# Kernel tuning notes

Hardware: AMD Instinct MI355X
Metric: run time of the kernel (lower is better)

## Reference

```python
import jax, jax.numpy as jnp
import numpy as np

B, L, T, D, F = 8, 12, 36, 1024, 3  # batch, local len, hist samples (n*tau), nodes, features
C = 32  # c_out


def setup_inputs() -> dict:
    key = jax.random.key(0)
    ks = jax.random.split(key, 8)
    s = 1.0 / np.sqrt(F)  # conv fan-in init scale
    return {
        "x_local": jax.random.normal(ks[0], (B, L, D, F), jnp.float32),
        "x_hist": jax.random.normal(ks[1], (B, L, T, D, F), jnp.float32),
        "Wq": jax.random.normal(ks[2], (C, F), jnp.float32) * s,
        "bq": jax.random.normal(ks[3], (C,), jnp.float32) * s,
        "Wm": jax.random.normal(ks[4], (C, F), jnp.float32) * s,
        "bm": jax.random.normal(ks[5], (C,), jnp.float32) * s,
        "Wc": jax.random.normal(ks[6], (C, F), jnp.float32) * s,
        "bc": jax.random.normal(ks[7], (C,), jnp.float32) * s,
    }


def reference(x_local, x_hist, Wq, bq, Wm, bm, Wc, bc):
    # 1x1 Conv2d/Conv3d over the feature channel F == pointwise linear in f.
    # torch permutes are absorbed into einsum axis ordering.
    q = jnp.einsum('bldf,cf->bcld', x_local, Wq) + bq[None, :, None, None]        # (B,C,L,D)
    m = jnp.einsum('bltdf,cf->bcltd', x_hist, Wm) + bm[None, :, None, None, None]  # (B,C,L,T,D)
    c = jnp.einsum('bltdf,cf->bcltd', x_hist, Wc) + bc[None, :, None, None, None]  # (B,C,L,T,D)
    mq = jnp.einsum('bcltd,bcld->bclt', m, q)                                     # scores (B,C,L,T)
    att = jax.nn.softmax(jax.nn.relu(mq), axis=-1)
    o = jnp.einsum('bclt,bcltd->bcld', att, c)                                    # memory read (B,C,L,D)
    return q + o
```

## Files before the change

kernel.cpp:

```cpp
#include <hip/hip_runtime.h>
#include <math.h>

#define BB 8
#define LL 12
#define TT 36
#define DD 1024
#define CC 32

__global__ __launch_bounds__(64) void k_Z(const float* __restrict__ xl,
                                          const float* __restrict__ xh,
                                          float* __restrict__ Zg) {
  const int blk  = blockIdx.x;
  const int bl   = blk / TT;
  const int lane = threadIdx.x;
  const float4* xh4 = (const float4*)xh + (size_t)blk * 768 + lane * 12;
  const float4* xl4 = (const float4*)xl + (size_t)bl  * 768 + lane * 12;

  float4 a4[12], b4[12];
  #pragma unroll
  for (int i = 0; i < 12; ++i) a4[i] = xh4[i];
  #pragma unroll
  for (int i = 0; i < 12; ++i) b4[i] = xl4[i];

  float Z00=0,Z01=0,Z02=0,Z10=0,Z11=0,Z12=0,Z20=0,Z21=0,Z22=0;
  float H0=0,H1=0,H2=0;
  const float* a = (const float*)a4;
  const float* b = (const float*)b4;
  #pragma unroll
  for (int k = 0; k < 16; ++k) {
    const float x0=a[k*3], x1=a[k*3+1], x2=a[k*3+2];
    const float y0=b[k*3], y1=b[k*3+1], y2=b[k*3+2];
    Z00 = fmaf(x0,y0,Z00); Z01 = fmaf(x0,y1,Z01); Z02 = fmaf(x0,y2,Z02);
    Z10 = fmaf(x1,y0,Z10); Z11 = fmaf(x1,y1,Z11); Z12 = fmaf(x1,y2,Z12);
    Z20 = fmaf(x2,y0,Z20); Z21 = fmaf(x2,y1,Z21); Z22 = fmaf(x2,y2,Z22);
    H0 += x0; H1 += x1; H2 += x2;
  }

  float v[12] = {Z00,Z01,Z02,Z10,Z11,Z12,Z20,Z21,Z22,H0,H1,H2};
  #pragma unroll
  for (int off = 32; off > 0; off >>= 1)
    #pragma unroll
    for (int j = 0; j < 12; ++j) v[j] += __shfl_down(v[j], off);

  if (lane == 0) {
    float4* o = (float4*)(Zg + (size_t)blk * 16);
    o[0] = make_float4(v[0], v[1], v[2],  v[3]);
    o[1] = make_float4(v[4], v[5], v[6],  v[7]);
    o[2] = make_float4(v[8], v[9], v[10], v[11]);
  }
}

__global__ __launch_bounds__(256) void k_soft(const float* __restrict__ xl,
                                              const float* __restrict__ Zg,
                                              const float* __restrict__ Wm,
                                              const float* __restrict__ bm,
                                              const float* __restrict__ Wq,
                                              const float* __restrict__ bq,
                                              const float* __restrict__ Wc,
                                              float* __restrict__ Pg) {
  __shared__ __align__(16) float ZS[TT * 16];
  __shared__ float S[TT][CC];
  __shared__ float xlp[4][3];
  __shared__ float mxv[CC], inv[CC];
  const int bl = blockIdx.x;
  const int tid = threadIdx.x;

  {
    const float4* src = (const float4*)(Zg + (size_t)bl * TT * 16);
    float4* dst = (float4*)ZS;
    if (tid < TT * 4) dst[tid] = src[tid];
  }
  {
    const float4* x4 = (const float4*)xl + (size_t)bl * 768 + tid * 3;
    const float4 a = x4[0], b = x4[1], c4 = x4[2];
    float s0 = a.x + a.w + b.z + c4.y;
    float s1 = a.y + b.x + b.w + c4.z;
    float s2 = a.z + b.y + c4.x + c4.w;
    #pragma unroll
    for (int off = 32; off > 0; off >>= 1) {
      s0 += __shfl_down(s0, off);
      s1 += __shfl_down(s1, off);
      s2 += __shfl_down(s2, off);
    }
    if ((tid & 63) == 0) {
      const int w = tid >> 6;
      xlp[w][0] = s0; xlp[w][1] = s1; xlp[w][2] = s2;
    }
  }
  __syncthreads();

  const float XL0 = (xlp[0][0]+xlp[1][0]) + (xlp[2][0]+xlp[3][0]);
  const float XL1 = (xlp[0][1]+xlp[1][1]) + (xlp[2][1]+xlp[3][1]);
  const float XL2 = (xlp[0][2]+xlp[1][2]) + (xlp[2][2]+xlp[3][2]);

  const int c = tid & 31;
  const float wm0 = Wm[c*3], wm1 = Wm[c*3+1], wm2 = Wm[c*3+2];
  const float wq0 = Wq[c*3], wq1 = Wq[c*3+1], wq2 = Wq[c*3+2];
  const float bqv = bq[c], bmv = bm[c];
  const float K = bmv * (fmaf(wq0, XL0, fmaf(wq1, XL1, wq2 * XL2)) + 1024.f * bqv);

  for (int idx = tid; idx < TT * CC; idx += 256) {
    const int t = idx >> 5;
    const float* z = &ZS[t * 16];
    float m = K;
    m = fmaf(wm0, fmaf(wq0, z[0], fmaf(wq1, z[1], fmaf(wq2, z[2], bqv * z[9]))),  m);
    m = fmaf(wm1, fmaf(wq0, z[3], fmaf(wq1, z[4], fmaf(wq2, z[5], bqv * z[10]))), m);
    m = fmaf(wm2, fmaf(wq0, z[6], fmaf(wq1, z[7], fmaf(wq2, z[8], bqv * z[11]))), m);
    S[t][c] = fmaxf(m, 0.f);
  }
  __syncthreads();

  if (tid < CC) {
    float mx = 0.f;
    #pragma unroll
    for (int t = 0; t < TT; ++t) mx = fmaxf(mx, S[t][tid]);
    float ssum = 0.f;
    #pragma unroll
    for (int t = 0; t < TT; ++t) ssum += __expf(S[t][tid] - mx);
    mxv[tid] = mx;
    inv[tid] = 1.f / ssum;
  }
  __syncthreads();

  const float wc0 = Wc[c*3], wc1 = Wc[c*3+1], wc2 = Wc[c*3+2];
  for (int idx = tid; idx < TT * CC; idx += 256) {
    const int t = idx >> 5;
    const float e = __expf(S[t][c] - mxv[c]) * inv[c];
    float* pp = Pg + (((size_t)bl * TT + t) * 3) * CC + c;
    pp[0]      = e * wc0;
    pp[CC]     = e * wc1;
    pp[2 * CC] = e * wc2;
  }
}

__global__ __launch_bounds__(512) void k_out(const float* __restrict__ xl,
                                             const float* __restrict__ xh,
                                             const float* __restrict__ Pg,
                                             const float* __restrict__ Wq,
                                             const float* __restrict__ bq,
                                             const float* __restrict__ bc,
                                             float* __restrict__ out) {
  __shared__ __align__(16) float4 PS[TT * 3 * 8];
  const int bl = blockIdx.x;
  const int b = bl / LL, l = bl % LL;
  const int dh = blockIdx.y;
  const int tid = threadIdx.x;
  const int lane = tid & 63;
  const int cq = tid >> 6;
  const int c0 = cq * 4;
  const int dg = dh * 64 + lane;

  {
    const float4* src = (const float4*)(Pg + (size_t)bl * TT * 3 * CC);
    for (int i = tid; i < TT * 3 * 8; i += 512) PS[i] = src[i];
  }
  __syncthreads();

  const float4* base = (const float4*)xh + (size_t)bl * TT * 768 + dg * 3;
  float4 buf[3][3];
  #pragma unroll
  for (int j = 0; j < 3; ++j)
    #pragma unroll
    for (int i = 0; i < 3; ++i) buf[j][i] = base[(size_t)j * 768 + i];

  float acc[4][4];
  #pragma unroll
  for (int u = 0; u < 4; ++u)
    #pragma unroll
    for (int dd = 0; dd < 4; ++dd) acc[u][dd] = 0.f;

  #pragma unroll
  for (int t = 0; t < TT; ++t) {
    const int sl = t % 3;
    float xv[12];
    {
      const float* x = (const float*)buf[sl];
      #pragma unroll
      for (int i = 0; i < 12; ++i) xv[i] = x[i];
    }
    if (t + 3 < TT) {
      const float4* p = base + (size_t)(t + 3) * 768;
      #pragma unroll
      for (int i = 0; i < 3; ++i) buf[sl][i] = p[i];
    }
    const float4 P0 = PS[(t * 3 + 0) * 8 + cq];
    const float4 P1 = PS[(t * 3 + 1) * 8 + cq];
    const float4 P2 = PS[(t * 3 + 2) * 8 + cq];
    const float p0[4] = {P0.x, P0.y, P0.z, P0.w};
    const float p1[4] = {P1.x, P1.y, P1.z, P1.w};
    const float p2[4] = {P2.x, P2.y, P2.z, P2.w};
    #pragma unroll
    for (int u = 0; u < 4; ++u)
      #pragma unroll
      for (int dd = 0; dd < 4; ++dd)
        acc[u][dd] = fmaf(p0[u], xv[dd*3],
                     fmaf(p1[u], xv[dd*3+1],
                     fmaf(p2[u], xv[dd*3+2], acc[u][dd])));
  }

  float4 ql[3];
  {
    const float4* xl4 = (const float4*)xl + (size_t)bl * 768 + dg * 3;
    #pragma unroll
    for (int i = 0; i < 3; ++i) ql[i] = xl4[i];
  }
  const float* y = (const float*)ql;
  #pragma unroll
  for (int u = 0; u < 4; ++u) {
    const int c = c0 + u;
    const float w0 = Wq[c*3], w1 = Wq[c*3+1], w2 = Wq[c*3+2];
    const float b0 = bq[c], bcv = bc[c];
    float4 o;
    o.x = acc[u][0] + bcv + fmaf(w0, y[0], fmaf(w1, y[1],  fmaf(w2, y[2],  b0)));
    o.y = acc[u][1] + bcv + fmaf(w0, y[3], fmaf(w1, y[4],  fmaf(w2, y[5],  b0)));
    o.z = acc[u][2] + bcv + fmaf(w0, y[6], fmaf(w1, y[7],  fmaf(w2, y[8],  b0)));
    o.w = acc[u][3] + bcv + fmaf(w0, y[9], fmaf(w1, y[10], fmaf(w2, y[11], b0)));
    *(float4*)(out + (((size_t)b * CC + c) * LL + l) * DD + dg * 4) = o;
  }
}

extern "C" void kernel_launch(void* const* d_in, const int* in_sizes, int n_in,
                              void* d_out, int out_size, void* d_ws, size_t ws_size,
                              hipStream_t stream) {
  const float* xl = (const float*)d_in[0];
  const float* xh = (const float*)d_in[1];
  const float* Wq = (const float*)d_in[2];
  const float* bq = (const float*)d_in[3];
  const float* Wm = (const float*)d_in[4];
  const float* bm = (const float*)d_in[5];
  const float* Wc = (const float*)d_in[6];
  const float* bc = (const float*)d_in[7];
  float* out = (float*)d_out;

  float* Zg = (float*)d_ws;
  float* Pg = Zg + (size_t)BB * LL * TT * 16;

  k_Z   <<<dim3(BB * LL * TT), 64,  0, stream>>>(xl, xh, Zg);
  k_soft<<<dim3(BB * LL),      256, 0, stream>>>(xl, Zg, Wm, bm, Wq, bq, Wc, Pg);
  k_out <<<dim3(BB * LL, 4),   512, 0, stream>>>(xl, xh, Pg, Wq, bq, bc, out);
}
```

Measured before the change: 134.2 us.

## Fuse softmax stage into output kernel and move xl sums into k_Z

Removes the separate softmax kernel. Each output block now recomputes the scores, softmax and P weights for its (b,l) in shared memory, and the per-(b,l) x_local channel sums are computed by the first k_Z block for that (b,l). The output grid doubles to 8 slices per (b,l) with 256 threads, so each thread still covers 4 channels by 4 nodes. This saves one launch and the round trip of P through global memory, at the cost of recomputing the softmax 8 times per (b,l) and adding three block barriers before the streaming loop.

```diff
diff --git a/kernel.cpp b/kernel.cpp
--- a/kernel.cpp
+++ b/kernel.cpp
@@ -9,7 +9,8 @@
 
 __global__ __launch_bounds__(64) void k_Z(const float* __restrict__ xl,
                                           const float* __restrict__ xh,
-                                          float* __restrict__ Zg) {
+                                          float* __restrict__ Zg,
+                                          float* __restrict__ XLg) {
   const int blk  = blockIdx.x;
   const int bl   = blk / TT;
   const int lane = threadIdx.x;
@@ -48,113 +49,96 @@
     o[1] = make_float4(v[4], v[5], v[6],  v[7]);
     o[2] = make_float4(v[8], v[9], v[10], v[11]);
   }
-}
-
-__global__ __launch_bounds__(256) void k_soft(const float* __restrict__ xl,
-                                              const float* __restrict__ Zg,
-                                              const float* __restrict__ Wm,
-                                              const float* __restrict__ bm,
-                                              const float* __restrict__ Wq,
-                                              const float* __restrict__ bq,
-                                              const float* __restrict__ Wc,
-                                              float* __restrict__ Pg) {
-  __shared__ __align__(16) float ZS[TT * 16];
-  __shared__ float S[TT][CC];
-  __shared__ float xlp[4][3];
-  __shared__ float mxv[CC], inv[CC];
-  const int bl = blockIdx.x;
-  const int tid = threadIdx.x;
-
-  {
-    const float4* src = (const float4*)(Zg + (size_t)bl * TT * 16);
-    float4* dst = (float4*)ZS;
-    if (tid < TT * 4) dst[tid] = src[tid];
-  }
-  {
-    const float4* x4 = (const float4*)xl + (size_t)bl * 768 + tid * 3;
-    const float4 a = x4[0], b = x4[1], c4 = x4[2];
-    float s0 = a.x + a.w + b.z + c4.y;
-    float s1 = a.y + b.x + b.w + c4.z;
-    float s2 = a.z + b.y + c4.x + c4.w;
+
+  if (blk == bl * TT) {
+    float s0=0.f, s1=0.f, s2=0.f;
+    #pragma unroll
+    for (int k = 0; k < 16; ++k) {
+      s0 += b[k*3]; s1 += b[k*3+1]; s2 += b[k*3+2];
+    }
     #pragma unroll
     for (int off = 32; off > 0; off >>= 1) {
       s0 += __shfl_down(s0, off);
       s1 += __shfl_down(s1, off);
       s2 += __shfl_down(s2, off);
     }
-    if ((tid & 63) == 0) {
-      const int w = tid >> 6;
-      xlp[w][0] = s0; xlp[w][1] = s1; xlp[w][2] = s2;
-    }
-  }
-  __syncthreads();
-
-  const float XL0 = (xlp[0][0]+xlp[1][0]) + (xlp[2][0]+xlp[3][0]);
-  const float XL1 = (xlp[0][1]+xlp[1][1]) + (xlp[2][1]+xlp[3][1]);
-  const float XL2 = (xlp[0][2]+xlp[1][2]) + (xlp[2][2]+xlp[3][2]);
-
-  const int c = tid & 31;
-  const float wm0 = Wm[c*3], wm1 = Wm[c*3+1], wm2 = Wm[c*3+2];
-  const float wq0 = Wq[c*3], wq1 = Wq[c*3+1], wq2 = Wq[c*3+2];
-  const float bqv = bq[c], bmv = bm[c];
-  const float K = bmv * (fmaf(wq0, XL0, fmaf(wq1, XL1, wq2 * XL2)) + 1024.f * bqv);
-
-  for (int idx = tid; idx < TT * CC; idx += 256) {
-    const int t = idx >> 5;
-    const float* z = &ZS[t * 16];
-    float m = K;
-    m = fmaf(wm0, fmaf(wq0, z[0], fmaf(wq1, z[1], fmaf(wq2, z[2], bqv * z[9]))),  m);
-    m = fmaf(wm1, fmaf(wq0, z[3], fmaf(wq1, z[4], fmaf(wq2, z[5], bqv * z[10]))), m);
-    m = fmaf(wm2, fmaf(wq0, z[6], fmaf(wq1, z[7], fmaf(wq2, z[8], bqv * z[11]))), m);
-    S[t][c] = fmaxf(m, 0.f);
-  }
-  __syncthreads();
-
-  if (tid < CC) {
-    float mx = 0.f;
-    #pragma unroll
-    for (int t = 0; t < TT; ++t) mx = fmaxf(mx, S[t][tid]);
-    float ssum = 0.f;
-    #pragma unroll
-    for (int t = 0; t < TT; ++t) ssum += __expf(S[t][tid] - mx);
-    mxv[tid] = mx;
-    inv[tid] = 1.f / ssum;
-  }
-  __syncthreads();
-
-  const float wc0 = Wc[c*3], wc1 = Wc[c*3+1], wc2 = Wc[c*3+2];
-  for (int idx = tid; idx < TT * CC; idx += 256) {
-    const int t = idx >> 5;
-    const float e = __expf(S[t][c] - mxv[c]) * inv[c];
-    float* pp = Pg + (((size_t)bl * TT + t) * 3) * CC + c;
-    pp[0]      = e * wc0;
-    pp[CC]     = e * wc1;
-    pp[2 * CC] = e * wc2;
+    if (lane == 0) {
+      XLg[bl*4+0] = s0; XLg[bl*4+1] = s1; XLg[bl*4+2] = s2;
+    }
   }
 }
 
-__global__ __launch_bounds__(512) void k_out(const float* __restrict__ xl,
+__global__ __launch_bounds__(256) void k_out(const float* __restrict__ xl,
                                              const float* __restrict__ xh,
-                                             const float* __restrict__ Pg,
+                                             const float* __restrict__ Zg,
+                                             const float* __restrict__ XLg,
+                                             const float* __restrict__ Wm,
+                                             const float* __restrict__ bm,
                                              const float* __restrict__ Wq,
                                              const float* __restrict__ bq,
+                                             const float* __restrict__ Wc,
                                              const float* __restrict__ bc,
                                              float* __restrict__ out) {
-  __shared__ __align__(16) float4 PS[TT * 3 * 8];
+  __shared__ __align__(16) float ZS[TT * 16];
+  __shared__ float S[TT][CC];
+  __shared__ __align__(16) float PS[TT * 3 * CC];
+  __shared__ float mxv[CC], inv[CC];
   const int bl = blockIdx.x;
   const int b = bl / LL, l = bl % LL;
   const int dh = blockIdx.y;
   const int tid = threadIdx.x;
-  const int lane = tid & 63;
-  const int cq = tid >> 6;
-  const int c0 = cq * 4;
-  const int dg = dh * 64 + lane;
+  const int c = tid & 31;
+
+  if (tid < TT * 4) ((float4*)ZS)[tid] = ((const float4*)(Zg + (size_t)bl * TT * 16))[tid];
+  __syncthreads();
 
   {
-    const float4* src = (const float4*)(Pg + (size_t)bl * TT * 3 * CC);
-    for (int i = tid; i < TT * 3 * 8; i += 512) PS[i] = src[i];
-  }
-  __syncthreads();
+    const float XL0 = XLg[bl*4+0], XL1 = XLg[bl*4+1], XL2 = XLg[bl*4+2];
+    const float wm0 = Wm[c*3], wm1 = Wm[c*3+1], wm2 = Wm[c*3+2];
+    const float wq0 = Wq[c*3], wq1 = Wq[c*3+1], wq2 = Wq[c*3+2];
+    const float bqv = bq[c], bmv = bm[c];
+    const float K = bmv * (fmaf(wq0, XL0, fmaf(wq1, XL1, wq2 * XL2)) + 1024.f * bqv);
+    for (int idx = tid; idx < TT * CC; idx += 256) {
+      const int t = idx >> 5;
+      const float* z = &ZS[t * 16];
+      float m = K;
+      m = fmaf(wm0, fmaf(wq0, z[0], fmaf(wq1, z[1], fmaf(wq2, z[2], bqv * z[9]))),  m);
+      m = fmaf(wm1, fmaf(wq0, z[3], fmaf(wq1, z[4], fmaf(wq2, z[5], bqv * z[10]))), m);
+      m = fmaf(wm2, fmaf(wq0, z[6], fmaf(wq1, z[7], fmaf(wq2, z[8], bqv * z[11]))), m);
+      S[t][c] = fmaxf(m, 0.f);
+    }
+  }
+  __syncthreads();
+
+  if (tid < CC) {
+    float mx = 0.f;
+    #pragma unroll
+    for (int t = 0; t < TT; ++t) mx = fmaxf(mx, S[t][tid]);
+    float ssum = 0.f;
+    #pragma unroll
+    for (int t = 0; t < TT; ++t) ssum += __expf(S[t][tid] - mx);
+    mxv[tid] = mx;
+    inv[tid] = 1.f / ssum;
+  }
+  __syncthreads();
+
+  {
+    const float wc0 = Wc[c*3], wc1 = Wc[c*3+1], wc2 = Wc[c*3+2];
+    const float mxc = mxv[c], invc = inv[c];
+    for (int idx = tid; idx < TT * CC; idx += 256) {
+      const int t = idx >> 5;
+      const float e = __expf(S[t][c] - mxc) * invc;
+      PS[(t*3+0)*CC + c] = e * wc0;
+      PS[(t*3+1)*CC + c] = e * wc1;
+      PS[(t*3+2)*CC + c] = e * wc2;
+    }
+  }
+  __syncthreads();
+
+  const int g  = tid & 31;
+  const int h5 = tid >> 5;
+  const int c0 = h5 * 4;
+  const int dg = dh * 32 + g;
 
   const float4* base = (const float4*)xh + (size_t)bl * TT * 768 + dg * 3;
   float4 buf[3][3];
@@ -169,6 +153,7 @@
     #pragma unroll
     for (int dd = 0; dd < 4; ++dd) acc[u][dd] = 0.f;
 
+  const float4* PS4 = (const float4*)PS;
   #pragma unroll
   for (int t = 0; t < TT; ++t) {
     const int sl = t % 3;
@@ -183,9 +168,9 @@
       #pragma unroll
       for (int i = 0; i < 3; ++i) buf[sl][i] = p[i];
     }
-    const float4 P0 = PS[(t * 3 + 0) * 8 + cq];
-    const float4 P1 = PS[(t * 3 + 1) * 8 + cq];
-    const float4 P2 = PS[(t * 3 + 2) * 8 + cq];
+    const float4 P0 = PS4[(t*3+0)*8 + h5];
+    const float4 P1 = PS4[(t*3+1)*8 + h5];
+    const float4 P2 = PS4[(t*3+2)*8 + h5];
     const float p0[4] = {P0.x, P0.y, P0.z, P0.w};
     const float p1[4] = {P1.x, P1.y, P1.z, P1.w};
     const float p2[4] = {P2.x, P2.y, P2.z, P2.w};
@@ -207,15 +192,15 @@
   const float* y = (const float*)ql;
   #pragma unroll
   for (int u = 0; u < 4; ++u) {
-    const int c = c0 + u;
-    const float w0 = Wq[c*3], w1 = Wq[c*3+1], w2 = Wq[c*3+2];
-    const float b0 = bq[c], bcv = bc[c];
+    const int cc = c0 + u;
+    const float w0 = Wq[cc*3], w1 = Wq[cc*3+1], w2 = Wq[cc*3+2];
+    const float b0 = bq[cc], bcv = bc[cc];
     float4 o;
     o.x = acc[u][0] + bcv + fmaf(w0, y[0], fmaf(w1, y[1],  fmaf(w2, y[2],  b0)));
     o.y = acc[u][1] + bcv + fmaf(w0, y[3], fmaf(w1, y[4],  fmaf(w2, y[5],  b0)));
     o.z = acc[u][2] + bcv + fmaf(w0, y[6], fmaf(w1, y[7],  fmaf(w2, y[8],  b0)));
     o.w = acc[u][3] + bcv + fmaf(w0, y[9], fmaf(w1, y[10], fmaf(w2, y[11], b0)));
-    *(float4*)(out + (((size_t)b * CC + c) * LL + l) * DD + dg * 4) = o;
+    *(float4*)(out + (((size_t)b * CC + cc) * LL + l) * DD + dg * 4) = o;
   }
 }
 
@@ -232,10 +217,10 @@
   const float* bc = (const float*)d_in[7];
   float* out = (float*)d_out;
 
-  float* Zg = (float*)d_ws;
-  float* Pg = Zg + (size_t)BB * LL * TT * 16;
-
-  k_Z   <<<dim3(BB * LL * TT), 64,  0, stream>>>(xl, xh, Zg);
-  k_soft<<<dim3(BB * LL),      256, 0, stream>>>(xl, Zg, Wm, bm, Wq, bq, Wc, Pg);
-  k_out <<<dim3(BB * LL, 4),   512, 0, stream>>>(xl, xh, Pg, Wq, bq, bc, out);
+  float* Zg  = (float*)d_ws;
+  float* XLg = Zg + (size_t)BB * LL * TT * 16;
+
+  k_Z  <<<dim3(BB * LL * TT), 64,  0, stream>>>(xl, xh, Zg, XLg);
+  k_out<<<dim3(BB * LL, 8),   256, 0, stream>>>(xl, xh, Zg, XLg, Wm, bm, Wq, bq,
+                                                Wc, bc, out);
 }
```

Result: faster. 124.1 us (-7.5%).
